# Performance work log

Measured on AMD Instinct MI355X. Metric: run time of the kernel, lower is better.

## Reference

```python
import jax, jax.numpy as jnp
import numpy as np

IN_FEATURES = 4096
OUT_FEATURES = 11008
N_TOKENS = 8192


def setup_inputs() -> dict:
    key = jax.random.key(0)
    kx, kw, kb = jax.random.split(key, 3)
    x = jax.random.normal(kx, (N_TOKENS, IN_FEATURES), dtype=jnp.float32)
    # nn.Linear weight: [out_features, in_features]
    bound = 1.0 / np.sqrt(IN_FEATURES)
    weight = jax.random.uniform(kw, (OUT_FEATURES, IN_FEATURES), dtype=jnp.float32,
                                minval=-bound, maxval=bound)
    bias = jax.random.uniform(kb, (OUT_FEATURES,), dtype=jnp.float32,
                              minval=-bound, maxval=bound)
    return {"x": x, "weight": weight, "bias": bias}


def reference(x, weight, bias):
    # Ternarize weights to {-1, 0, +1} then standard dense matmul + bias.
    ternary_w = jnp.sign(weight)  # [out, in]
    return jnp.matmul(x, ternary_w.T) + bias  # [n_tokens, out]
```

## Files before the change

kernel.cpp:

```cpp
#include <hip/hip_runtime.h>
#include <stdint.h>

#define M_DIM 8192
#define N_DIM 11008
#define K_DIM 4096

#define BM 256
#define BN 256
#define BK 64
#define NT (K_DIM / BK)
#define GRID_M (M_DIM / BM)
#define GRID_N (N_DIM / BN)
#define NWG (GRID_M * GRID_N)

#define BUF (BM * BK)
#define NRING 4

typedef int i32x4 __attribute__((ext_vector_type(4)));

__device__ __forceinline__ void gload16(const int8_t* src, int8_t* dst) {
    __builtin_amdgcn_global_load_lds(
        (const __attribute__((address_space(1))) uint32_t*)src,
        (__attribute__((address_space(3))) uint32_t*)dst, 16, 0, 0);
}


__global__ __launch_bounds__(256) void quant_x_kernel(
    const float* __restrict__ x, int8_t* __restrict__ xq, float* __restrict__ sinv)
{
    const int wave = blockIdx.x * 4 + (threadIdx.x >> 6);
    const int lane = threadIdx.x & 63;
    const float* row = x + (size_t)wave * K_DIM;

    float4 v[16];
    float mx = 0.0f;
    #pragma unroll
    for (int j = 0; j < 16; ++j) {
        v[j] = *(const float4*)(row + (j * 64 + lane) * 4);
        mx = fmaxf(mx, fmaxf(fmaxf(fabsf(v[j].x), fabsf(v[j].y)),
                             fmaxf(fabsf(v[j].z), fabsf(v[j].w))));
    }
    #pragma unroll
    for (int off = 32; off > 0; off >>= 1)
        mx = fmaxf(mx, __shfl_xor(mx, off));
    if (mx < 1e-30f) mx = 1e-30f;
    const float s = 127.0f / mx;

    int8_t* orow = xq + (size_t)wave * K_DIM;
    #pragma unroll
    for (int j = 0; j < 16; ++j) {
        int a = (int)__builtin_rintf(v[j].x * s);
        int b = (int)__builtin_rintf(v[j].y * s);
        int c = (int)__builtin_rintf(v[j].z * s);
        int d = (int)__builtin_rintf(v[j].w * s);
        uint32_t p = (uint32_t)(a & 0xFF) | ((uint32_t)(b & 0xFF) << 8) |
                     ((uint32_t)(c & 0xFF) << 16) | ((uint32_t)(d & 0xFF) << 24);
        *(uint32_t*)(orow + (j * 64 + lane) * 4) = p;
    }
    if (lane == 0) sinv[wave] = mx / 127.0f;
}


__global__ __launch_bounds__(256) void sign_w_kernel(
    const float* __restrict__ w, int8_t* __restrict__ wq, long long n16)
{
    long long i = (long long)blockIdx.x * blockDim.x + threadIdx.x;
    const long long stride = (long long)gridDim.x * blockDim.x;
    for (; i < n16; i += stride) {
        const float* src = w + i * 16;
        uint32_t pk[4];
        #pragma unroll
        for (int q = 0; q < 4; ++q) {
            float4 f = *(const float4*)(src + q * 4);
            int a = (f.x > 0.f) ? 1 : ((f.x < 0.f) ? -1 : 0);
            int b = (f.y > 0.f) ? 1 : ((f.y < 0.f) ? -1 : 0);
            int c = (f.z > 0.f) ? 1 : ((f.z < 0.f) ? -1 : 0);
            int d = (f.w > 0.f) ? 1 : ((f.w < 0.f) ? -1 : 0);
            pk[q] = (uint32_t)(a & 0xFF) | ((uint32_t)(b & 0xFF) << 8) |
                    ((uint32_t)(c & 0xFF) << 16) | ((uint32_t)(d & 0xFF) << 24);
        }
        *(i32x4*)(wq + i * 16) = (i32x4){(int)pk[0], (int)pk[1], (int)pk[2], (int)pk[3]};
    }
}


__global__ __launch_bounds__(1024, 4) void ternary_gemm_i8(
    const int8_t* __restrict__ A, const int8_t* __restrict__ B,
    const float* __restrict__ bias, const float* __restrict__ sinv,
    float* __restrict__ out)
{
    extern __shared__ int8_t lds[];
    int8_t* As = lds;
    int8_t* Bs = lds + NRING * BUF;

    const int tid  = threadIdx.x;
    const int lane = tid & 63;
    const int wid  = tid >> 6;
    const int wr   = wid >> 2;
    const int wc   = wid & 3;
    const int l15  = lane & 15;
    const int l4   = lane >> 4;

    const int bid = blockIdx.x;
    const int swz = (bid & 7) * (NWG / 8) + (bid >> 3);
    const int bm  = swz / GRID_N;
    const int bn  = swz % GRID_N;
    const long brow = (long)bm * BM;
    const long bcol = (long)bn * BN;

    const int rowt = tid >> 2;
    const int ssrc = (tid & 3) ^ ((tid >> 3) & 3);
    const int8_t* pA = A + (size_t)(brow + rowt) * K_DIM + ssrc * 16;
    const int8_t* pB = B + (size_t)(bcol + rowt) * K_DIM + ssrc * 16;

    auto stageAB = [&](int t, int bslot) {
        gload16(pA + (size_t)t * BK, As + bslot * BUF + tid * 16);
        gload16(pB + (size_t)t * BK, Bs + bslot * BUF + tid * 16);
    };

    const int slot = l4 ^ ((l15 >> 1) & 3);
    const int aOff = (wr * 64 + l15) * 64 + slot * 16;
    const int bOff = (wc * 64 + l15) * 64 + slot * 16;

    i32x4 acc[4][4];
    #pragma unroll
    for (int m = 0; m < 4; ++m)
        #pragma unroll
        for (int n = 0; n < 4; ++n) acc[m][n] = (i32x4){0, 0, 0, 0};

    stageAB(0, 0); stageAB(1, 1); stageAB(2, 2);
    asm volatile("s_waitcnt vmcnt(4)" ::: "memory");
    __builtin_amdgcn_s_barrier();
    __builtin_amdgcn_sched_barrier(0);

    for (int t = 0; t < NT; ++t) {
        const int b = t & 3;

        i32x4 ar[4], br[4];
        #pragma unroll
        for (int m = 0; m < 4; ++m)
            ar[m] = *(const i32x4*)(As + b * BUF + m * 1024 + aOff);
        #pragma unroll
        for (int n = 0; n < 4; ++n)
            br[n] = *(const i32x4*)(Bs + b * BUF + n * 1024 + bOff);

        if (t + 3 < NT) stageAB(t + 3, (t + 3) & 3);

        __builtin_amdgcn_s_setprio(1);
        #pragma unroll
        for (int m = 0; m < 4; ++m)
            #pragma unroll
            for (int n = 0; n < 4; ++n)
                acc[m][n] = __builtin_amdgcn_mfma_i32_16x16x64_i8(ar[m], br[n], acc[m][n], 0, 0, 0);
        __builtin_amdgcn_s_setprio(0);
        __builtin_amdgcn_sched_barrier(0);

        if (t <= NT - 4)      { asm volatile("s_waitcnt vmcnt(4)" ::: "memory"); }
        else if (t == NT - 3) { asm volatile("s_waitcnt vmcnt(2)" ::: "memory"); }
        else                  { asm volatile("s_waitcnt vmcnt(0)" ::: "memory"); }
        __builtin_amdgcn_s_barrier();
        __builtin_amdgcn_sched_barrier(0);
    }

    int   cols[4];
    float bv[4];
    #pragma unroll
    for (int n = 0; n < 4; ++n) {
        cols[n] = (int)bcol + wc * 64 + n * 16 + l15;
        bv[n] = bias[cols[n]];
    }
    #pragma unroll
    for (int m = 0; m < 4; ++m) {
        const size_t row0 = (size_t)brow + wr * 64 + m * 16 + l4 * 4;
        float s0 = sinv[row0], s1 = sinv[row0 + 1], s2 = sinv[row0 + 2], s3 = sinv[row0 + 3];
        #pragma unroll
        for (int n = 0; n < 4; ++n) {
            out[(row0 + 0) * N_DIM + cols[n]] = (float)acc[m][n][0] * s0 + bv[n];
            out[(row0 + 1) * N_DIM + cols[n]] = (float)acc[m][n][1] * s1 + bv[n];
            out[(row0 + 2) * N_DIM + cols[n]] = (float)acc[m][n][2] * s2 + bv[n];
            out[(row0 + 3) * N_DIM + cols[n]] = (float)acc[m][n][3] * s3 + bv[n];
        }
    }
}


__global__ void naive_kernel(const float* __restrict__ x, const float* __restrict__ w,
                             const float* __restrict__ bias, float* __restrict__ out) {
    long long o = (long long)blockIdx.x * blockDim.x + threadIdx.x;
    if (o >= (long long)M_DIM * N_DIM) return;
    int row = (int)(o / N_DIM), col = (int)(o % N_DIM);
    float s = 0.0f;
    const float* xr = x + (size_t)row * K_DIM;
    const float* wr = w + (size_t)col * K_DIM;
    for (int k = 0; k < K_DIM; ++k) {
        float wv = wr[k];
        s += (wv > 0.0f) ? xr[k] : ((wv < 0.0f) ? -xr[k] : 0.0f);
    }
    out[o] = s + bias[col];
}


extern "C" void kernel_launch(void* const* d_in, const int* in_sizes, int n_in,
                              void* d_out, int out_size, void* d_ws, size_t ws_size,
                              hipStream_t stream) {
    const float* x    = (const float*)d_in[0];
    const float* w    = (const float*)d_in[1];
    const float* bias = (const float*)d_in[2];
    float* out        = (float*)d_out;

    const size_t xq_bytes = (size_t)M_DIM * K_DIM;
    const size_t wq_bytes = (size_t)N_DIM * K_DIM;
    const size_t si_bytes = (size_t)M_DIM * sizeof(float);

    if (ws_size >= xq_bytes + wq_bytes + si_bytes) {
        int8_t* xq   = (int8_t*)d_ws;
        int8_t* wq   = (int8_t*)((char*)d_ws + xq_bytes);
        float*  sinv = (float*)((char*)d_ws + xq_bytes + wq_bytes);

        quant_x_kernel<<<M_DIM / 4, 256, 0, stream>>>(x, xq, sinv);
        const long long n16 = ((long long)N_DIM * K_DIM) / 16;
        sign_w_kernel<<<2048, 256, 0, stream>>>(w, wq, n16);

        const int lds_bytes = NRING * 2 * BUF;
        hipFuncSetAttribute(reinterpret_cast<const void*>(ternary_gemm_i8),
                            hipFuncAttributeMaxDynamicSharedMemorySize, lds_bytes);
        ternary_gemm_i8<<<NWG, 1024, lds_bytes, stream>>>(xq, wq, bias, sinv, out);
    } else {
        const long long total = (long long)M_DIM * N_DIM;
        naive_kernel<<<(int)((total + 255) / 256), 256, 0, stream>>>(x, w, bias, out);
    }
}
```

Before: 463.8 us.

## Replace 4-deep BK=64 LDS ring with double-buffered BK=128 stages

Switches the int8 GEMM main loop from a 4-slot ring of 64-wide K tiles with a 3-tile prefetch depth to a double-buffered scheme of 128-wide K stages, each split into two 64-wide halves. This halves the number of barriers and waitcnts per K sweep, and each stage issues all its loads before computing on the current buffer. In exchange, prefetch depth drops to one stage, and every iteration ends with a full vmcnt(0) wait, which may expose more global-load latency. LDS footprint stays at 128 KB.

```diff
diff --git a/kernel.cpp b/kernel.cpp
--- a/kernel.cpp
+++ b/kernel.cpp
@@ -7,14 +7,14 @@
 
 #define BM 256
 #define BN 256
-#define BK 64
-#define NT (K_DIM / BK)
+#define BKS 128
+#define NS (K_DIM / BKS)
 #define GRID_M (M_DIM / BM)
 #define GRID_N (N_DIM / BN)
 #define NWG (GRID_M * GRID_N)
 
-#define BUF (BM * BK)
-#define NRING 4
+#define HBUF 16384
+#define SBUF (2 * HBUF)
 
 typedef int i32x4 __attribute__((ext_vector_type(4)));
 
@@ -91,7 +91,7 @@
 {
     extern __shared__ int8_t lds[];
     int8_t* As = lds;
-    int8_t* Bs = lds + NRING * BUF;
+    int8_t* Bs = lds + 2 * SBUF;
 
     const int tid  = threadIdx.x;
     const int lane = tid & 63;
@@ -113,9 +113,13 @@
     const int8_t* pA = A + (size_t)(brow + rowt) * K_DIM + ssrc * 16;
     const int8_t* pB = B + (size_t)(bcol + rowt) * K_DIM + ssrc * 16;
 
-    auto stageAB = [&](int t, int bslot) {
-        gload16(pA + (size_t)t * BK, As + bslot * BUF + tid * 16);
-        gload16(pB + (size_t)t * BK, Bs + bslot * BUF + tid * 16);
+    auto stageS = [&](int S, int sl) {
+        #pragma unroll
+        for (int h = 0; h < 2; ++h) {
+            const size_t koff = (size_t)S * BKS + (size_t)h * 64;
+            gload16(pA + koff, As + sl * SBUF + h * HBUF + tid * 16);
+            gload16(pB + koff, Bs + sl * SBUF + h * HBUF + tid * 16);
+        }
     };
 
     const int slot = l4 ^ ((l15 >> 1) & 3);
@@ -128,36 +132,42 @@
         #pragma unroll
         for (int n = 0; n < 4; ++n) acc[m][n] = (i32x4){0, 0, 0, 0};
 
-    stageAB(0, 0); stageAB(1, 1); stageAB(2, 2);
-    asm volatile("s_waitcnt vmcnt(4)" ::: "memory");
+    stageS(0, 0);
+    asm volatile("s_waitcnt vmcnt(0)" ::: "memory");
     __builtin_amdgcn_s_barrier();
     __builtin_amdgcn_sched_barrier(0);
 
-    for (int t = 0; t < NT; ++t) {
-        const int b = t & 3;
-
-        i32x4 ar[4], br[4];
-        #pragma unroll
-        for (int m = 0; m < 4; ++m)
-            ar[m] = *(const i32x4*)(As + b * BUF + m * 1024 + aOff);
-        #pragma unroll
-        for (int n = 0; n < 4; ++n)
-            br[n] = *(const i32x4*)(Bs + b * BUF + n * 1024 + bOff);
-
-        if (t + 3 < NT) stageAB(t + 3, (t + 3) & 3);
-
-        __builtin_amdgcn_s_setprio(1);
-        #pragma unroll
-        for (int m = 0; m < 4; ++m)
+    for (int S = 0; S < NS; ++S) {
+        const int c = S & 1;
+        const int8_t* Ac = As + c * SBUF;
+        const int8_t* Bc = Bs + c * SBUF;
+
+        if (S + 1 < NS) stageS(S + 1, c ^ 1);
+
+        #pragma unroll
+        for (int h = 0; h < 2; ++h) {
+            const int8_t* Ah = Ac + h * HBUF;
+            const int8_t* Bh = Bc + h * HBUF;
+            i32x4 ar[4], br[4];
             #pragma unroll
             for (int n = 0; n < 4; ++n)
-                acc[m][n] = __builtin_amdgcn_mfma_i32_16x16x64_i8(ar[m], br[n], acc[m][n], 0, 0, 0);
-        __builtin_amdgcn_s_setprio(0);
+                br[n] = *(const i32x4*)(Bh + n * 1024 + bOff);
+            #pragma unroll
+            for (int m = 0; m < 4; ++m)
+                ar[m] = *(const i32x4*)(Ah + m * 1024 + aOff);
+
+            __builtin_amdgcn_s_setprio(1);
+            #pragma unroll
+            for (int m = 0; m < 4; ++m)
+                #pragma unroll
+                for (int n = 0; n < 4; ++n)
+                    acc[m][n] = __builtin_amdgcn_mfma_i32_16x16x64_i8(
+                        ar[m], br[n], acc[m][n], 0, 0, 0);
+            __builtin_amdgcn_s_setprio(0);
+        }
         __builtin_amdgcn_sched_barrier(0);
 
-        if (t <= NT - 4)      { asm volatile("s_waitcnt vmcnt(4)" ::: "memory"); }
-        else if (t == NT - 3) { asm volatile("s_waitcnt vmcnt(2)" ::: "memory"); }
-        else                  { asm volatile("s_waitcnt vmcnt(0)" ::: "memory"); }
+        asm volatile("s_waitcnt vmcnt(0)" ::: "memory");
         __builtin_amdgcn_s_barrier();
         __builtin_amdgcn_sched_barrier(0);
     }
@@ -221,7 +231,7 @@
         const long long n16 = ((long long)N_DIM * K_DIM) / 16;
         sign_w_kernel<<<2048, 256, 0, stream>>>(w, wq, n16);
 
-        const int lds_bytes = NRING * 2 * BUF;
+        const int lds_bytes = 4 * SBUF;
         hipFuncSetAttribute(reinterpret_cast<const void*>(ternary_gemm_i8),
                             hipFuncAttributeMaxDynamicSharedMemorySize, lds_bytes);
         ternary_gemm_i8<<<NWG, 1024, lds_bytes, stream>>>(xq, wq, bias, sinv, out);
```

After: 468.1 us. No clear change (+0.9%).
